# Performance work log

Measured on AMD Instinct MI355X. Metric: run time of the kernel, lower is better.

The kernel has to match this reference:

```python
import jax, jax.numpy as jnp
import numpy as np

N_NODES = 100000
N_EDGES = 800000
IN_CH = 128
HID = 128
OUT_CH = 64


def setup_inputs() -> dict:
    key = jax.random.key(0)
    ks = jax.random.split(key, 8)
    x = jax.random.normal(ks[0], (N_NODES, IN_CH), dtype=jnp.float32)
    edge_index = jax.random.randint(ks[1], (2, N_EDGES), 0, N_NODES, dtype=jnp.int64)
    # GCNConv weights (Glorot) and zero biases
    def glorot(k, fan_in, fan_out):
        s = jnp.sqrt(6.0 / (fan_in + fan_out))
        return jax.random.uniform(k, (fan_in, fan_out), jnp.float32, -s, s)
    return {
        "x": x,
        "edge_index": edge_index,
        "W1": glorot(ks[2], IN_CH, HID), "b1": jnp.zeros((HID,), jnp.float32),
        "W2": glorot(ks[3], HID, HID),   "b2": jnp.zeros((HID,), jnp.float32),
        "W3": glorot(ks[4], HID, OUT_CH), "b3": jnp.zeros((OUT_CH,), jnp.float32),
    }


def _gcn_conv(h, W, b, src, dst, norm, self_norm, n_nodes):
    """PyG GCNConv: out = D^-1/2 (A+I) D^-1/2 (h W) + b.
    Self-loop contribution added densely (self_norm = dinv^2) to avoid
    appending N extra edges."""
    h = h @ W  # [N, F_out]
    msg = h[src] * norm[:, None]  # [E, F_out] gathered + normalized messages
    agg = jax.ops.segment_sum(msg, dst, num_segments=n_nodes)
    return agg + h * self_norm[:, None] + b


def reference(x, edge_index, W1, b1, W2, b2, W3, b3):
    n_nodes = x.shape[0]
    src = edge_index[0]
    dst = edge_index[1]
    # degrees with self-loops (edge weights = 1)
    deg = jax.ops.segment_sum(jnp.ones_like(src, dtype=x.dtype), dst,
                              num_segments=n_nodes) + 1.0
    dinv = jax.lax.rsqrt(deg)
    norm = dinv[src] * dinv[dst]   # per-edge symmetric normalization
    self_norm = dinv * dinv        # normalization of the i->i self loop

    h = jax.nn.relu(_gcn_conv(x, W1, b1, src, dst, norm, self_norm, n_nodes))
    # dropout is identity in eval mode (training=False)
    h = jax.nn.relu(_gcn_conv(h, W2, b2, src, dst, norm, self_norm, n_nodes))
    out = _gcn_conv(h, W3, b3, src, dst, norm, self_norm, n_nodes)
    return out
```

## Files before the change

kernel.cpp:

```cpp
#include <hip/hip_runtime.h>


#define IN_CH 128

typedef __attribute__((ext_vector_type(8))) short bf16x8;
typedef __attribute__((ext_vector_type(4))) float f32x4;

__device__ inline unsigned short f2bf_rne(float f) {
    unsigned u = __float_as_uint(f);
    unsigned r = (u + 0x7FFFu + ((u >> 16) & 1u)) >> 16;
    return (unsigned short)r;
}
__device__ inline float bf2f(unsigned short h) {
    return __uint_as_float(((unsigned)h) << 16);
}
__device__ inline float bf2f_lo(unsigned m) {
    return __uint_as_float(m << 16);
}
__device__ inline float bf2f_hi(unsigned m) {
    return __uint_as_float(m & 0xffff0000u);
}

__global__ __launch_bounds__(256) void cnt_k(const int* __restrict__ dst,
                                             int* __restrict__ cnt, int E) {
    int e = blockIdx.x * 256 + threadIdx.x;
    if (e < E) atomicAdd(&cnt[dst[e]], 1);
}

__global__ __launch_bounds__(256) void scan1_k(const int* __restrict__ cnt,
                                               int* __restrict__ bsum,
                                               float* __restrict__ dinv, int N) {
    __shared__ int s[256];
    int tid = threadIdx.x;
    int i = blockIdx.x * 256 + tid;
    int vr = (i < N) ? cnt[i] : 0;
    if (i < N) dinv[i] = rsqrtf((float)vr + 1.0f);
    s[tid] = (i < N) ? ((vr + 3) & ~3) : 0;
    __syncthreads();
    for (int off = 128; off > 0; off >>= 1) {
        if (tid < off) s[tid] += s[tid + off];
        __syncthreads();
    }
    if (tid == 0) bsum[blockIdx.x] = s[0];
}

__global__ __launch_bounds__(512) void scan2_k(int* __restrict__ bsum, int nb) {
    __shared__ int s[512];
    __shared__ int carry_s;
    int tid = threadIdx.x;
    if (tid == 0) carry_s = 0;
    __syncthreads();
    for (int base = 0; base < nb; base += 512) {
        int c = carry_s;
        int i = base + tid;
        int v = (i < nb) ? bsum[i] : 0;
        s[tid] = v;
        __syncthreads();
        for (int off = 1; off < 512; off <<= 1) {
            int t = (tid >= off) ? s[tid - off] : 0;
            __syncthreads();
            s[tid] += t;
            __syncthreads();
        }
        if (i < nb) bsum[i] = s[tid] - v + c;
        __syncthreads();
        if (tid == 0) carry_s = c + s[511];
        __syncthreads();
    }
}

__global__ __launch_bounds__(256) void scan3_k(const int* __restrict__ cnt,
                                               const int* __restrict__ bsum,
                                               int* __restrict__ rowstart,
                                               int* __restrict__ cur, int N) {
    __shared__ int s[256];
    int tid = threadIdx.x;
    int i = blockIdx.x * 256 + tid;
    int v = (i < N) ? ((cnt[i] + 3) & ~3) : 0;
    s[tid] = v;
    __syncthreads();
    for (int off = 1; off < 256; off <<= 1) {
        int t = (tid >= off) ? s[tid - off] : 0;
        __syncthreads();
        s[tid] += t;
        __syncthreads();
    }
    if (i < N) {
        int st = s[tid] - v + bsum[blockIdx.x];
        rowstart[i] = st;
        cur[i] = st;
        if (i == N - 1) rowstart[N] = st + v;
    }
}

__device__ inline void convw_one(const float* W, unsigned short* hi, int FOUT, int id) {
    int n = id >> 7, k = id & 127;
    hi[id] = f2bf_rne(W[k * FOUT + n]);
}

__global__ __launch_bounds__(256) void fill_conv_k(
    const int* __restrict__ src, const int* __restrict__ dst,
    const float* __restrict__ dinv, int* __restrict__ cur,
    int2* __restrict__ pairs, int E, int fillBlocks, int rangeSz,
    const float* __restrict__ W1, const float* __restrict__ W2,
    const float* __restrict__ W3,
    unsigned short* __restrict__ W1h, unsigned short* __restrict__ W2h,
    unsigned short* __restrict__ W3h) {
    if ((int)blockIdx.x < fillBlocks) {
        const int range = blockIdx.x & 7;
        const int lo = range * rangeSz;
        const int hi = lo + rangeSz;
        const int e0 = (blockIdx.x >> 3) * 1024 + threadIdx.x * 4;
        if (e0 >= E) return;
        int s[4], d[4];
        if (e0 + 4 <= E) {
            int4 s4 = *(const int4*)(src + e0);
            int4 d4 = *(const int4*)(dst + e0);
            s[0] = s4.x; s[1] = s4.y; s[2] = s4.z; s[3] = s4.w;
            d[0] = d4.x; d[1] = d4.y; d[2] = d4.z; d[3] = d4.w;
        } else {
#pragma unroll
            for (int k = 0; k < 4; ++k) {
                s[k] = (e0 + k < E) ? src[e0 + k] : 0;
                d[k] = (e0 + k < E) ? dst[e0 + k] : -1;
            }
        }
#pragma unroll
        for (int k = 0; k < 4; ++k) {
            if (d[k] >= lo && d[k] < hi) {
                float nrm = dinv[s[k]] * dinv[d[k]];
                int pos = atomicAdd(&cur[d[k]], 1);
                pairs[pos] = make_int2(s[k] * 256, __float_as_int(nrm));
            }
        }
    } else {
        int id = (blockIdx.x - fillBlocks) * 256 + threadIdx.x;
        if (id < 16384) convw_one(W1, W1h, 128, id);
        else if (id < 32768) convw_one(W2, W2h, 128, id - 16384);
        else if (id < 40960) convw_one(W3, W3h, 64, id - 32768);
    }
}

__device__ inline bf16x8 cvt8(const float* __restrict__ p) {
    float4 v0 = *(const float4*)p;
    float4 v1 = *(const float4*)(p + 4);
    bf16x8 h;
    h[0] = (short)f2bf_rne(v0.x); h[1] = (short)f2bf_rne(v0.y);
    h[2] = (short)f2bf_rne(v0.z); h[3] = (short)f2bf_rne(v0.w);
    h[4] = (short)f2bf_rne(v1.x); h[5] = (short)f2bf_rne(v1.y);
    h[6] = (short)f2bf_rne(v1.z); h[7] = (short)f2bf_rne(v1.w);
    return h;
}

template <int FOUT, bool AF32>
__global__ __launch_bounds__(256) void mfma_gemm(const float* __restrict__ Af,
                                                 const unsigned short* __restrict__ Ahi,
                                                 const unsigned short* __restrict__ Bhi,
                                                 unsigned short* __restrict__ Thi,
                                                 int N) {
    constexpr int NCT = FOUT / 16;
    constexpr int BSTRIDE = 136;
    constexpr int CSTRIDE = FOUT + 8;
    constexpr int BU = FOUT * BSTRIDE;
    constexpr int CU = 64 * CSTRIDE;
    constexpr int SMEMU = (BU > CU) ? BU : CU;
    __shared__ unsigned short smem[SMEMU];

    const int tid = threadIdx.x;
    const int wv = tid >> 6, lane = tid & 63;
    const int quad = lane >> 4, l16 = lane & 15;
    const int row0 = blockIdx.x * 64 + wv * 16;

#pragma unroll
    for (int it = 0; it < FOUT / 16; ++it) {
        int i = it * 256 + tid;
        int r = i >> 4, c = (i & 15) * 8;
        *(bf16x8*)(&smem[r * BSTRIDE + c]) = *(const bf16x8*)(Bhi + (size_t)r * 128 + c);
    }
    __syncthreads();

    f32x4 acc[NCT];
#pragma unroll
    for (int ct = 0; ct < NCT; ++ct)
        acc[ct] = (f32x4){0.f, 0.f, 0.f, 0.f};

    const int ra = AF32 ? min(row0 + l16, N - 1) : (row0 + l16);

#pragma unroll
    for (int ks = 0; ks < 4; ++ks) {
        const int ko = ks * 32 + quad * 8;
        bf16x8 ah;
        if (AF32) {
            ah = cvt8(Af + (size_t)ra * 128 + ko);
        } else {
            ah = *(const bf16x8*)(Ahi + (size_t)ra * 128 + ko);
        }
#pragma unroll
        for (int ct = 0; ct < NCT; ++ct) {
            bf16x8 bh = *(const bf16x8*)(&smem[(ct * 16 + l16) * BSTRIDE + ko]);
            acc[ct] = __builtin_amdgcn_mfma_f32_16x16x32_bf16(ah, bh, acc[ct], 0, 0, 0);
        }
    }

    __syncthreads();
    const int lrow = wv * 16 + quad * 4;
#pragma unroll
    for (int ct = 0; ct < NCT; ++ct) {
        const int col = ct * 16 + l16;
#pragma unroll
        for (int r = 0; r < 4; ++r)
            smem[(lrow + r) * CSTRIDE + col] = f2bf_rne(acc[ct][r]);
    }
    __syncthreads();
    constexpr int CH = FOUT / 8;
#pragma unroll
    for (int i = 0; i < 64 * CH / 256; ++i) {
        int ci = i * 256 + tid;
        int r = ci / CH, c = (ci % CH) * 8;
        int grow = blockIdx.x * 64 + r;
        if (grow < N)
            *(uint4*)(Thi + (size_t)grow * FOUT + c) = *(const uint4*)&smem[r * CSTRIDE + c];
    }
}

template <int FOUT, bool SPLIT>
__global__ __launch_bounds__(256) void gather_k(const int* __restrict__ rowstart,
                                                const int2* __restrict__ pairs,
                                                const float* __restrict__ dinv,
                                                const unsigned short* __restrict__ Thi,
                                                const float* __restrict__ bias,
                                                float* __restrict__ out,
                                                unsigned short* __restrict__ outHi,
                                                int N) {
    const int wave = threadIdx.x >> 6;
    const int lane = threadIdx.x & 63;
    const int row = blockIdx.x * 4 + wave;
    if (row >= N) return;

    const int start = rowstart[row];
    const int end = rowstart[row + 1];
    const float dr = dinv[row];
    const char* tbase = (const char*)Thi;

    if (FOUT == 128) {
        const int laneB = lane * 4;
        unsigned sh = *(const unsigned*)(tbase + (size_t)row * 256 + laneB);
        float2 bb = *(const float2*)(bias + lane * 2);
        float ax = bb.x + bf2f_lo(sh) * dr * dr;
        float ay = bb.y + bf2f_hi(sh) * dr * dr;

        for (int j = start; j < end; j += 4) {
            int4 p01 = *(const int4*)(pairs + j);
            int4 p23 = *(const int4*)(pairs + j + 2);
            unsigned m0 = *(const unsigned*)(tbase + (unsigned)p01.x + laneB);
            unsigned m1 = *(const unsigned*)(tbase + (unsigned)p01.z + laneB);
            unsigned m2 = *(const unsigned*)(tbase + (unsigned)p23.x + laneB);
            unsigned m3 = *(const unsigned*)(tbase + (unsigned)p23.z + laneB);
            float n0 = __int_as_float(p01.y), n1 = __int_as_float(p01.w);
            float n2 = __int_as_float(p23.y), n3 = __int_as_float(p23.w);
            ax += n0 * bf2f_lo(m0); ay += n0 * bf2f_hi(m0);
            ax += n1 * bf2f_lo(m1); ay += n1 * bf2f_hi(m1);
            ax += n2 * bf2f_lo(m2); ay += n2 * bf2f_hi(m2);
            ax += n3 * bf2f_lo(m3); ay += n3 * bf2f_hi(m3);
        }

        if (SPLIT) {
            float vx = fmaxf(ax, 0.f), vy = fmaxf(ay, 0.f);
            ushort2 h;
            h.x = f2bf_rne(vx);
            h.y = f2bf_rne(vy);
            *(ushort2*)(outHi + (size_t)row * 128 + lane * 2) = h;
        } else {
            float2 o; o.x = ax; o.y = ay;
            *(float2*)(out + (size_t)row * 128 + lane * 2) = o;
        }
    } else {
        const int laneB = lane * 2;
        float acc = bias[lane] +
                    bf2f(*(const unsigned short*)(tbase + (size_t)row * 128 + laneB)) * dr * dr;

        for (int j = start; j < end; j += 4) {
            int4 p01 = *(const int4*)(pairs + j);
            int4 p23 = *(const int4*)(pairs + j + 2);
            float m0 = bf2f(*(const unsigned short*)(tbase + ((unsigned)p01.x >> 1) + laneB));
            float m1 = bf2f(*(const unsigned short*)(tbase + ((unsigned)p01.z >> 1) + laneB));
            float m2 = bf2f(*(const unsigned short*)(tbase + ((unsigned)p23.x >> 1) + laneB));
            float m3 = bf2f(*(const unsigned short*)(tbase + ((unsigned)p23.z >> 1) + laneB));
            acc += __int_as_float(p01.y) * m0 + __int_as_float(p01.w) * m1 +
                   __int_as_float(p23.y) * m2 + __int_as_float(p23.w) * m3;
        }
        out[(size_t)row * FOUT + lane] = acc;
    }
}

extern "C" void kernel_launch(void* const* d_in, const int* in_sizes, int n_in,
                              void* d_out, int out_size, void* d_ws, size_t ws_size,
                              hipStream_t stream) {
    const float* x  = (const float*)d_in[0];
    const int* eidx = (const int*)d_in[1];
    const float* W1 = (const float*)d_in[2];
    const float* b1 = (const float*)d_in[3];
    const float* W2 = (const float*)d_in[4];
    const float* b2 = (const float*)d_in[5];
    const float* W3 = (const float*)d_in[6];
    const float* b3 = (const float*)d_in[7];
    float* out = (float*)d_out;

    const int N = in_sizes[0] / IN_CH;
    const int E = in_sizes[1] / 2;
    const int* src = eidx;
    const int* dst = eidx + E;
    const int Npad = ((N + 127) / 128) * 128;
    const int nb = (N + 255) / 256;
    const int Emax = E + 3 * N;

    auto align = [](size_t v) { return (v + 255) / 256 * 256; };
    char* p = (char*)d_ws;
    int* cnt = (int*)p;            p += align((size_t)N * 4);
    int* rowstart = (int*)p;       p += align((size_t)(N + 1) * 4);
    int* cur = (int*)p;            p += align((size_t)N * 4);
    int* bsum = (int*)p;           p += align((size_t)nb * 4);
    float* dinv = (float*)p;       p += align((size_t)N * 4);
    int2* pairs = (int2*)p;        p += align((size_t)Emax * 8);
    unsigned short* Ahi = (unsigned short*)p;  p += align((size_t)Npad * 128 * 2);
    unsigned short* Thi = (unsigned short*)p;  p += align((size_t)Npad * 128 * 2);
    unsigned short* W1h = (unsigned short*)p;  p += align(128 * 128 * 2);
    unsigned short* W2h = (unsigned short*)p;  p += align(128 * 128 * 2);
    unsigned short* W3h = (unsigned short*)p;

    hipMemsetAsync(cnt, 0, (size_t)N * 4, stream);
    hipMemsetAsync(pairs, 0, (size_t)Emax * 8, stream);
    cnt_k<<<(E + 255) / 256, 256, 0, stream>>>(dst, cnt, E);
    scan1_k<<<nb, 256, 0, stream>>>(cnt, bsum, dinv, N);
    scan2_k<<<1, 512, 0, stream>>>(bsum, nb);
    scan3_k<<<nb, 256, 0, stream>>>(cnt, bsum, rowstart, cur, N);
    const int chunks = (E + 1023) / 1024;
    const int fillBlocks = chunks * 8;
    const int rangeSz = (N + 7) / 8;
    fill_conv_k<<<fillBlocks + 160, 256, 0, stream>>>(src, dst, dinv, cur, pairs,
                                                      E, fillBlocks, rangeSz,
                                                      W1, W2, W3, W1h, W2h, W3h);

    const int gemm_blocks = (N + 63) / 64;
    const int gather_blocks = (N + 3) / 4;

    mfma_gemm<128, true><<<gemm_blocks, 256, 0, stream>>>(x, nullptr, W1h, Thi, N);
    gather_k<128, true><<<gather_blocks, 256, 0, stream>>>(rowstart, pairs, dinv, Thi,
                                                           b1, nullptr, Ahi, N);
    mfma_gemm<128, false><<<gemm_blocks, 256, 0, stream>>>(nullptr, Ahi, W2h, Thi, N);
    gather_k<128, true><<<gather_blocks, 256, 0, stream>>>(rowstart, pairs, dinv, Thi,
                                                           b2, nullptr, Ahi, N);
    mfma_gemm<64, false><<<gemm_blocks, 256, 0, stream>>>(nullptr, Ahi, W3h, Thi, N);
    gather_k<64, false><<<gather_blocks, 256, 0, stream>>>(rowstart, pairs, dinv, Thi,
                                                           b3, out, nullptr, N);
}
```

Baseline: 336.6 us.

## Fold self-loops into CSR and process two rows per wave with prefetched pairs

The self-loop term becomes an explicit CSR entry written during the fill kernel, and row padding changes from multiples of 4 to multiples of 8. The gather kernel now has each wave handle two adjacent rows. It interleaves their 8-edge chunks and software-prefetches the next pair block, aiming to raise memory-level parallelism and hide gather latency. The cost is more padding entries (zero-weight gathers of row 0), a larger pairs buffer, and higher register pressure.

```diff
diff --git a/kernel.cpp b/kernel.cpp
--- a/kernel.cpp
+++ b/kernel.cpp
@@ -35,7 +35,7 @@
     int i = blockIdx.x * 256 + tid;
     int vr = (i < N) ? cnt[i] : 0;
     if (i < N) dinv[i] = rsqrtf((float)vr + 1.0f);
-    s[tid] = (i < N) ? ((vr + 3) & ~3) : 0;
+    s[tid] = (i < N) ? ((vr + 8) & ~7) : 0;
     __syncthreads();
     for (int off = 128; off > 0; off >>= 1) {
         if (tid < off) s[tid] += s[tid + off];
@@ -76,7 +76,7 @@
     __shared__ int s[256];
     int tid = threadIdx.x;
     int i = blockIdx.x * 256 + tid;
-    int v = (i < N) ? ((cnt[i] + 3) & ~3) : 0;
+    int v = (i < N) ? ((cnt[i] + 8) & ~7) : 0;
     s[tid] = v;
     __syncthreads();
     for (int off = 1; off < 256; off <<= 1) {
@@ -101,7 +101,8 @@
 __global__ __launch_bounds__(256) void fill_conv_k(
     const int* __restrict__ src, const int* __restrict__ dst,
     const float* __restrict__ dinv, int* __restrict__ cur,
-    int2* __restrict__ pairs, int E, int fillBlocks, int rangeSz,
+    int2* __restrict__ pairs, int E, int N, int fillBlocks, int selfBlocks,
+    int rangeSz,
     const float* __restrict__ W1, const float* __restrict__ W2,
     const float* __restrict__ W3,
     unsigned short* __restrict__ W1h, unsigned short* __restrict__ W2h,
@@ -133,8 +134,15 @@
                 pairs[pos] = make_int2(s[k] * 256, __float_as_int(nrm));
             }
         }
+    } else if ((int)blockIdx.x < fillBlocks + selfBlocks) {
+        int i = (blockIdx.x - fillBlocks) * 256 + threadIdx.x;
+        if (i < N) {
+            float di = dinv[i];
+            int pos = atomicAdd(&cur[i], 1);
+            pairs[pos] = make_int2(i * 256, __float_as_int(di * di));
+        }
     } else {
-        int id = (blockIdx.x - fillBlocks) * 256 + threadIdx.x;
+        int id = (blockIdx.x - fillBlocks - selfBlocks) * 256 + threadIdx.x;
         if (id < 16384) convw_one(W1, W1h, 128, id);
         else if (id < 32768) convw_one(W2, W2h, 128, id - 16384);
         else if (id < 40960) convw_one(W3, W3h, 64, id - 32768);
@@ -223,10 +231,67 @@
     }
 }
 
+struct Pairs4 { int4 p0, p1, p2, p3; };
+
+__device__ inline Pairs4 ldpairs(const int2* __restrict__ pairs, int j) {
+    Pairs4 r;
+    r.p0 = *(const int4*)(pairs + j);
+    r.p1 = *(const int4*)(pairs + j + 2);
+    r.p2 = *(const int4*)(pairs + j + 4);
+    r.p3 = *(const int4*)(pairs + j + 6);
+    return r;
+}
+
+__device__ inline void ldrows128(const char* __restrict__ tbase, int laneB,
+                                 const Pairs4& P, unsigned m[8]) {
+    m[0] = *(const unsigned*)(tbase + (unsigned)P.p0.x + laneB);
+    m[1] = *(const unsigned*)(tbase + (unsigned)P.p0.z + laneB);
+    m[2] = *(const unsigned*)(tbase + (unsigned)P.p1.x + laneB);
+    m[3] = *(const unsigned*)(tbase + (unsigned)P.p1.z + laneB);
+    m[4] = *(const unsigned*)(tbase + (unsigned)P.p2.x + laneB);
+    m[5] = *(const unsigned*)(tbase + (unsigned)P.p2.z + laneB);
+    m[6] = *(const unsigned*)(tbase + (unsigned)P.p3.x + laneB);
+    m[7] = *(const unsigned*)(tbase + (unsigned)P.p3.z + laneB);
+}
+
+__device__ inline void fma8_128(const Pairs4& P, const unsigned m[8],
+                                float& ax, float& ay) {
+    float n0 = __int_as_float(P.p0.y), n1 = __int_as_float(P.p0.w);
+    float n2 = __int_as_float(P.p1.y), n3 = __int_as_float(P.p1.w);
+    float n4 = __int_as_float(P.p2.y), n5 = __int_as_float(P.p2.w);
+    float n6 = __int_as_float(P.p3.y), n7 = __int_as_float(P.p3.w);
+    ax += n0 * bf2f_lo(m[0]); ay += n0 * bf2f_hi(m[0]);
+    ax += n1 * bf2f_lo(m[1]); ay += n1 * bf2f_hi(m[1]);
+    ax += n2 * bf2f_lo(m[2]); ay += n2 * bf2f_hi(m[2]);
+    ax += n3 * bf2f_lo(m[3]); ay += n3 * bf2f_hi(m[3]);
+    ax += n4 * bf2f_lo(m[4]); ay += n4 * bf2f_hi(m[4]);
+    ax += n5 * bf2f_lo(m[5]); ay += n5 * bf2f_hi(m[5]);
+    ax += n6 * bf2f_lo(m[6]); ay += n6 * bf2f_hi(m[6]);
+    ax += n7 * bf2f_lo(m[7]); ay += n7 * bf2f_hi(m[7]);
+}
+
+__device__ inline void ldrows64(const char* __restrict__ tbase, int laneB,
+                                const Pairs4& P, float m[8]) {
+    m[0] = bf2f(*(const unsigned short*)(tbase + ((unsigned)P.p0.x >> 1) + laneB));
+    m[1] = bf2f(*(const unsigned short*)(tbase + ((unsigned)P.p0.z >> 1) + laneB));
+    m[2] = bf2f(*(const unsigned short*)(tbase + ((unsigned)P.p1.x >> 1) + laneB));
+    m[3] = bf2f(*(const unsigned short*)(tbase + ((unsigned)P.p1.z >> 1) + laneB));
+    m[4] = bf2f(*(const unsigned short*)(tbase + ((unsigned)P.p2.x >> 1) + laneB));
+    m[5] = bf2f(*(const unsigned short*)(tbase + ((unsigned)P.p2.z >> 1) + laneB));
+    m[6] = bf2f(*(const unsigned short*)(tbase + ((unsigned)P.p3.x >> 1) + laneB));
+    m[7] = bf2f(*(const unsigned short*)(tbase + ((unsigned)P.p3.z >> 1) + laneB));
+}
+
+__device__ inline void fma8_64(const Pairs4& P, const float m[8], float& acc) {
+    acc += __int_as_float(P.p0.y) * m[0] + __int_as_float(P.p0.w) * m[1] +
+           __int_as_float(P.p1.y) * m[2] + __int_as_float(P.p1.w) * m[3] +
+           __int_as_float(P.p2.y) * m[4] + __int_as_float(P.p2.w) * m[5] +
+           __int_as_float(P.p3.y) * m[6] + __int_as_float(P.p3.w) * m[7];
+}
+
 template <int FOUT, bool SPLIT>
 __global__ __launch_bounds__(256) void gather_k(const int* __restrict__ rowstart,
                                                 const int2* __restrict__ pairs,
-                                                const float* __restrict__ dinv,
                                                 const unsigned short* __restrict__ Thi,
                                                 const float* __restrict__ bias,
                                                 float* __restrict__ out,
@@ -234,62 +299,118 @@
                                                 int N) {
     const int wave = threadIdx.x >> 6;
     const int lane = threadIdx.x & 63;
-    const int row = blockIdx.x * 4 + wave;
-    if (row >= N) return;
-
-    const int start = rowstart[row];
-    const int end = rowstart[row + 1];
-    const float dr = dinv[row];
+    const int rowA = blockIdx.x * 8 + wave * 2;
+    if (rowA >= N) return;
+    const int rowB = rowA + 1;
+    const bool hasB = rowB < N;
+
+    int2 se = *(const int2*)(rowstart + rowA);
+    const int startA = se.x, endA = se.y;
+    const int startB = endA;
+    const int endB = hasB ? rowstart[rowA + 2] : startB;
     const char* tbase = (const char*)Thi;
+
+    int itA = (endA - startA) >> 3;
+    int itB = (endB - startB) >> 3;
+    const int c = min(itA, itB);
 
     if (FOUT == 128) {
         const int laneB = lane * 4;
-        unsigned sh = *(const unsigned*)(tbase + (size_t)row * 256 + laneB);
         float2 bb = *(const float2*)(bias + lane * 2);
-        float ax = bb.x + bf2f_lo(sh) * dr * dr;
-        float ay = bb.y + bf2f_hi(sh) * dr * dr;
-
-        for (int j = start; j < end; j += 4) {
-            int4 p01 = *(const int4*)(pairs + j);
-            int4 p23 = *(const int4*)(pairs + j + 2);
-            unsigned m0 = *(const unsigned*)(tbase + (unsigned)p01.x + laneB);
-            unsigned m1 = *(const unsigned*)(tbase + (unsigned)p01.z + laneB);
-            unsigned m2 = *(const unsigned*)(tbase + (unsigned)p23.x + laneB);
-            unsigned m3 = *(const unsigned*)(tbase + (unsigned)p23.z + laneB);
-            float n0 = __int_as_float(p01.y), n1 = __int_as_float(p01.w);
-            float n2 = __int_as_float(p23.y), n3 = __int_as_float(p23.w);
-            ax += n0 * bf2f_lo(m0); ay += n0 * bf2f_hi(m0);
-            ax += n1 * bf2f_lo(m1); ay += n1 * bf2f_hi(m1);
-            ax += n2 * bf2f_lo(m2); ay += n2 * bf2f_hi(m2);
-            ax += n3 * bf2f_lo(m3); ay += n3 * bf2f_hi(m3);
+        float axA = bb.x, ayA = bb.y, axB = bb.x, ayB = bb.y;
+
+        Pairs4 PA = ldpairs(pairs, startA);
+        Pairs4 PB = {};
+        if (hasB) PB = ldpairs(pairs, startB);
+        int jA = startA, jB = startB;
+
+        for (int t = 0; t < c; ++t) {
+            unsigned mA[8], mB[8];
+            ldrows128(tbase, laneB, PA, mA);
+            ldrows128(tbase, laneB, PB, mB);
+            jA += 8; jB += 8;
+            Pairs4 QA = ldpairs(pairs, jA);
+            Pairs4 QB = ldpairs(pairs, jB);
+            fma8_128(PA, mA, axA, ayA);
+            fma8_128(PB, mB, axB, ayB);
+            PA = QA; PB = QB;
+        }
+        for (int t = c; t < itA; ++t) {
+            unsigned mA[8];
+            ldrows128(tbase, laneB, PA, mA);
+            jA += 8;
+            Pairs4 QA = ldpairs(pairs, jA);
+            fma8_128(PA, mA, axA, ayA);
+            PA = QA;
+        }
+        for (int t = c; t < itB; ++t) {
+            unsigned mB[8];
+            ldrows128(tbase, laneB, PB, mB);
+            jB += 8;
+            Pairs4 QB = ldpairs(pairs, jB);
+            fma8_128(PB, mB, axB, ayB);
+            PB = QB;
         }
 
         if (SPLIT) {
-            float vx = fmaxf(ax, 0.f), vy = fmaxf(ay, 0.f);
-            ushort2 h;
-            h.x = f2bf_rne(vx);
-            h.y = f2bf_rne(vy);
-            *(ushort2*)(outHi + (size_t)row * 128 + lane * 2) = h;
+            ushort2 hA;
+            hA.x = f2bf_rne(fmaxf(axA, 0.f));
+            hA.y = f2bf_rne(fmaxf(ayA, 0.f));
+            *(ushort2*)(outHi + (size_t)rowA * 128 + lane * 2) = hA;
+            if (hasB) {
+                ushort2 hB;
+                hB.x = f2bf_rne(fmaxf(axB, 0.f));
+                hB.y = f2bf_rne(fmaxf(ayB, 0.f));
+                *(ushort2*)(outHi + (size_t)rowB * 128 + lane * 2) = hB;
+            }
         } else {
-            float2 o; o.x = ax; o.y = ay;
-            *(float2*)(out + (size_t)row * 128 + lane * 2) = o;
+            float2 oA; oA.x = axA; oA.y = ayA;
+            *(float2*)(out + (size_t)rowA * 128 + lane * 2) = oA;
+            if (hasB) {
+                float2 oB; oB.x = axB; oB.y = ayB;
+                *(float2*)(out + (size_t)rowB * 128 + lane * 2) = oB;
+            }
         }
     } else {
         const int laneB = lane * 2;
-        float acc = bias[lane] +
-                    bf2f(*(const unsigned short*)(tbase + (size_t)row * 128 + laneB)) * dr * dr;
-
-        for (int j = start; j < end; j += 4) {
-            int4 p01 = *(const int4*)(pairs + j);
-            int4 p23 = *(const int4*)(pairs + j + 2);
-            float m0 = bf2f(*(const unsigned short*)(tbase + ((unsigned)p01.x >> 1) + laneB));
-            float m1 = bf2f(*(const unsigned short*)(tbase + ((unsigned)p01.z >> 1) + laneB));
-            float m2 = bf2f(*(const unsigned short*)(tbase + ((unsigned)p23.x >> 1) + laneB));
-            float m3 = bf2f(*(const unsigned short*)(tbase + ((unsigned)p23.z >> 1) + laneB));
-            acc += __int_as_float(p01.y) * m0 + __int_as_float(p01.w) * m1 +
-                   __int_as_float(p23.y) * m2 + __int_as_float(p23.w) * m3;
-        }
-        out[(size_t)row * FOUT + lane] = acc;
+        const float bb = bias[lane];
+        float accA = bb, accB = bb;
+
+        Pairs4 PA = ldpairs(pairs, startA);
+        Pairs4 PB = {};
+        if (hasB) PB = ldpairs(pairs, startB);
+        int jA = startA, jB = startB;
+
+        for (int t = 0; t < c; ++t) {
+            float mA[8], mB[8];
+            ldrows64(tbase, laneB, PA, mA);
+            ldrows64(tbase, laneB, PB, mB);
+            jA += 8; jB += 8;
+            Pairs4 QA = ldpairs(pairs, jA);
+            Pairs4 QB = ldpairs(pairs, jB);
+            fma8_64(PA, mA, accA);
+            fma8_64(PB, mB, accB);
+            PA = QA; PB = QB;
+        }
+        for (int t = c; t < itA; ++t) {
+            float mA[8];
+            ldrows64(tbase, laneB, PA, mA);
+            jA += 8;
+            Pairs4 QA = ldpairs(pairs, jA);
+            fma8_64(PA, mA, accA);
+            PA = QA;
+        }
+        for (int t = c; t < itB; ++t) {
+            float mB[8];
+            ldrows64(tbase, laneB, PB, mB);
+            jB += 8;
+            Pairs4 QB = ldpairs(pairs, jB);
+            fma8_64(PB, mB, accB);
+            PB = QB;
+        }
+
+        out[(size_t)rowA * FOUT + lane] = accA;
+        if (hasB) out[(size_t)rowB * FOUT + lane] = accB;
     }
 }
 
@@ -312,7 +433,7 @@
     const int* dst = eidx + E;
     const int Npad = ((N + 127) / 128) * 128;
     const int nb = (N + 255) / 256;
-    const int Emax = E + 3 * N;
+    const int Emax = E + 8 * N + 24;
 
     auto align = [](size_t v) { return (v + 255) / 256 * 256; };
     char* p = (char*)d_ws;
@@ -336,21 +457,22 @@
     scan3_k<<<nb, 256, 0, stream>>>(cnt, bsum, rowstart, cur, N);
     const int chunks = (E + 1023) / 1024;
     const int fillBlocks = chunks * 8;
+    const int selfBlocks = (N + 255) / 256;
     const int rangeSz = (N + 7) / 8;
-    fill_conv_k<<<fillBlocks + 160, 256, 0, stream>>>(src, dst, dinv, cur, pairs,
-                                                      E, fillBlocks, rangeSz,
-                                                      W1, W2, W3, W1h, W2h, W3h);
+    fill_conv_k<<<fillBlocks + selfBlocks + 160, 256, 0, stream>>>(
+        src, dst, dinv, cur, pairs, E, N, fillBlocks, selfBlocks, rangeSz,
+        W1, W2, W3, W1h, W2h, W3h);
 
     const int gemm_blocks = (N + 63) / 64;
-    const int gather_blocks = (N + 3) / 4;
+    const int gather_blocks = (N + 7) / 8;
 
     mfma_gemm<128, true><<<gemm_blocks, 256, 0, stream>>>(x, nullptr, W1h, Thi, N);
-    gather_k<128, true><<<gather_blocks, 256, 0, stream>>>(rowstart, pairs, dinv, Thi,
+    gather_k<128, true><<<gather_blocks, 256, 0, stream>>>(rowstart, pairs, Thi,
                                                            b1, nullptr, Ahi, N);
     mfma_gemm<128, false><<<gemm_blocks, 256, 0, stream>>>(nullptr, Ahi, W2h, Thi, N);
-    gather_k<128, true><<<gather_blocks, 256, 0, stream>>>(rowstart, pairs, dinv, Thi,
+    gather_k<128, true><<<gather_blocks, 256, 0, stream>>>(rowstart, pairs, Thi,
                                                            b2, nullptr, Ahi, N);
     mfma_gemm<64, false><<<gemm_blocks, 256, 0, stream>>>(nullptr, Ahi, W3h, Thi, N);
-    gather_k<64, false><<<gather_blocks, 256, 0, stream>>>(rowstart, pairs, dinv, Thi,
+    gather_k<64, false><<<gather_blocks, 256, 0, stream>>>(rowstart, pairs, Thi,
                                                            b3, out, nullptr, N);
 }
```

Result: slower. 350.6 us (+4.2%).
